# Kernel optimization log

Measured on AMD Instinct MI355X. Metric: run time of the kernel, lower is better.

Reference implementation:

```python
import jax, jax.numpy as jnp
import numpy as np

D = 1024          # d_input_feature
GCN_OUTS = [1024, 512, 256]
DEC_OUTS = [512, 1024, 1024]  # reversed[1:] + [d_input_feature]
EPS = 1e-3        # keras LayerNormalization default epsilon


def _ln(x, gamma, beta):
    m = jnp.mean(x, axis=-1, keepdims=True)
    v = jnp.mean(jnp.square(x - m), axis=-1, keepdims=True)
    return gamma * (x - m) * jax.lax.rsqrt(v + EPS) + beta


def _gcn(x, A, W, b, act):
    # message passing with dense adjacency: act((A @ x) @ W + b)
    h = jnp.einsum('bij,bjd->bid', A, x)
    return act(h @ W + b)


def setup_inputs() -> dict:
    key = jax.random.key(0)
    ks = jax.random.split(key, 40)
    B, DG, DC, NTT = 16384, 772, 100, 128
    inp = {
        't_1': jax.random.randint(ks[0], (B,), 0, NTT),
        'g_1': jax.random.normal(ks[1], (B, DG), jnp.float32),
        'c_1': jax.random.normal(ks[2], (B, DC), jnp.float32),
        'A_1': jax.random.uniform(ks[3], (B, 3, 3), jnp.float32),
        't_2': jax.random.randint(ks[4], (B,), 0, NTT),
        'g_2': jax.random.normal(ks[5], (B, DG), jnp.float32),
        'c_2': jax.random.normal(ks[6], (B, DC), jnp.float32),
        'A_2': jax.random.uniform(ks[7], (B, 3, 3), jnp.float32),
        'embed': jax.random.normal(ks[8], (NTT, D), jnp.float32) * 0.02,
        'Wt': jax.random.normal(ks[9], (D, D), jnp.float32) / np.sqrt(D),
        'bt': jnp.zeros((D,), jnp.float32),
        'Wg': jax.random.normal(ks[10], (DG, D), jnp.float32) / np.sqrt(DG),
        'bg': jnp.zeros((D,), jnp.float32),
        'Wc': jax.random.normal(ks[11], (DC, D), jnp.float32) / np.sqrt(DC),
        'bc': jnp.zeros((D,), jnp.float32),
        'ln_t_g': jnp.ones((D,), jnp.float32), 'ln_t_b': jnp.zeros((D,), jnp.float32),
        'ln_g_g': jnp.ones((D,), jnp.float32), 'ln_g_b': jnp.zeros((D,), jnp.float32),
        'ln_c_g': jnp.ones((D,), jnp.float32), 'ln_c_b': jnp.zeros((D,), jnp.float32),
    }
    d_in = D
    for i, d_out in enumerate(GCN_OUTS):
        inp[f'enc_W{i}'] = jax.random.normal(ks[12 + i], (d_in, d_out), jnp.float32) / np.sqrt(d_in)
        inp[f'enc_b{i}'] = jnp.zeros((d_out,), jnp.float32)
        d_in = d_out
    for i, d_out in enumerate(DEC_OUTS):
        inp[f'dec_W{i}'] = jax.random.normal(ks[20 + i], (d_in, d_out), jnp.float32) / np.sqrt(d_in)
        inp[f'dec_b{i}'] = jnp.zeros((d_out,), jnp.float32)
        d_in = d_out
    return inp


def _branch(t, g, c, embed, Wt, bt, Wg, bg, Wc, bc,
            ln_t_g, ln_t_b, ln_g_g, ln_g_b, ln_c_g, ln_c_b):
    te = embed[t]                               # [B, D]
    te = jax.nn.relu(te @ Wt + bt)
    ge = jax.nn.relu(g @ Wg + bg)
    ce = jax.nn.relu(c @ Wc + bc)
    te = _ln(te, ln_t_g, ln_t_b)
    ge = _ln(ge, ln_g_g, ln_g_b)
    ce = _ln(ce, ln_c_g, ln_c_b)
    return jnp.stack([te, ge, ce], axis=1)      # [B, 3, D]


def _encoder(X, A, enc):
    x = X
    for W, b in enc:
        x = _gcn(x, A, W, b, jax.nn.relu)
    return x


def _decoder(Z, A, dec):
    x = Z
    for W, b in dec:
        x = _gcn(x, A, W, b, jax.nn.silu)       # swish
    return x


def reference(t_1, g_1, c_1, A_1, t_2, g_2, c_2, A_2,
              embed, Wt, bt, Wg, bg, Wc, bc,
              ln_t_g, ln_t_b, ln_g_g, ln_g_b, ln_c_g, ln_c_b,
              enc_W0, enc_b0, enc_W1, enc_b1, enc_W2, enc_b2,
              dec_W0, dec_b0, dec_W1, dec_b1, dec_W2, dec_b2):
    enc = [(enc_W0, enc_b0), (enc_W1, enc_b1), (enc_W2, enc_b2)]
    dec = [(dec_W0, dec_b0), (dec_W1, dec_b1), (dec_W2, dec_b2)]
    bargs = (embed, Wt, bt, Wg, bg, Wc, bc,
             ln_t_g, ln_t_b, ln_g_g, ln_g_b, ln_c_g, ln_c_b)

    X_1 = _branch(t_1, g_1, c_1, *bargs)
    X_2 = _branch(t_2, g_2, c_2, *bargs)
    Z_1 = _encoder(X_1, A_1, enc)
    Z_2 = _encoder(X_2, A_2, enc)
    Z_loss = jnp.square(Z_1 - Z_2)              # [B, 3, 256]

    # GAE reconstruction path (recomputes X per the original code)
    X_h_1 = _decoder(Z_1, A_1, dec)
    X_h_2 = _decoder(Z_2, A_2, dec)
    X_loss = (jnp.square(X_1 - X_h_1) + jnp.square(X_2 - X_h_2)) / 2.0  # [B, 3, D]
    return Z_loss, X_loss
```

## Files before the change

### kernel.cpp

```cpp
#include <hip/hip_runtime.h>


typedef __attribute__((ext_vector_type(8))) short s16x8;
typedef __attribute__((ext_vector_type(4))) short s16x4;
typedef __attribute__((ext_vector_type(4))) float f32x4;

#define DEV static __device__ __forceinline__

DEV float b2f(ushort u) { return __builtin_bit_cast(float, (unsigned)u << 16); }
DEV ushort f2b(float f) {
  unsigned x = __builtin_bit_cast(unsigned, f);
  unsigned r = x + 0x7fffu + ((x >> 16) & 1u);
  return (ushort)(r >> 16);
}

typedef const __attribute__((address_space(1))) void* gas_ptr;
typedef __attribute__((address_space(3))) void* las_ptr;

template<int ACT>
__global__ __launch_bounds__(512, 2) void gemm256(
    const ushort* __restrict__ A, const ushort* __restrict__ BT,
    const float* __restrict__ bias, ushort* __restrict__ C,
    int M, int N, int K)
{
  __shared__ __align__(16) ushort ldsbuf[65536];
  char* Lb = (char*)ldsbuf;

  const int tid = threadIdx.x, lane = tid & 63, w = tid >> 6;
  const int wm = w >> 2, wn = w & 3;

  const int gx  = gridDim.x;
  const int nwg = gx * gridDim.y;
  const int wid = blockIdx.y * gx + blockIdx.x;
  const int q   = nwg >> 3;
  const int Lw  = (wid & 7) * q + (wid >> 3);
  const int bn  = Lw % gx;
  const int bm  = Lw / gx;

  const ushort* Abase = A  + (size_t)bm * 256 * K;
  const ushort* Bbase = BT + (size_t)bn * 256 * K;
  const int T = K >> 6;

  const int srow = w * 8 + (lane >> 3);
  const int scol = (((lane & 7) ^ (lane >> 3)) << 3);

#define STAGE(buf, m, half, Gb, k0)                                          \
  {                                                                          \
    _Pragma("unroll") for (int _j = 0; _j < 2; ++_j) {                       \
      const ushort* _src = (Gb) + (size_t)((half)*128 + _j*64 + srow) * K    \
                           + (k0) + scol;                                    \
      ushort* _dst = (ushort*)(Lb + ((buf)*2 + (m)) * 32768                  \
                               + ((half)*128 + _j*64 + w*8) * 128);          \
      __builtin_amdgcn_global_load_lds((gas_ptr)_src, (las_ptr)_dst, 16,0,0);\
    }                                                                        \
  }

  const int lr = lane & 15, lk = lane >> 4;

#define READ_A(dst, c, mh)                                                   \
  _Pragma("unroll") for (int _i = 0; _i < 4; ++_i)                           \
    _Pragma("unroll") for (int _kk = 0; _kk < 2; ++_kk) {                    \
      const int _r   = (mh)*128 + wm*64 + _i*16 + lr;                        \
      const int _cbb = _kk*64 + lk*16;                                       \
      dst[_i][_kk] = *(const s16x8*)(Lb + ((c)*2 + 0)*32768 + _r*128         \
                                     + (_cbb ^ ((_r & 7) << 4)));            \
    }
#define READ_B(dst, c, nh)                                                   \
  _Pragma("unroll") for (int _p = 0; _p < 2; ++_p)                           \
    _Pragma("unroll") for (int _kk = 0; _kk < 2; ++_kk) {                    \
      const int _r   = (nh)*128 + wn*32 + _p*16 + lr;                        \
      const int _cbb = _kk*64 + lk*16;                                       \
      dst[_p][_kk] = *(const s16x8*)(Lb + ((c)*2 + 1)*32768 + _r*128         \
                                     + (_cbb ^ ((_r & 7) << 4)));            \
    }

#define MFMA_Q(mh, nh)                                                       \
  _Pragma("unroll") for (int _i = 0; _i < 4; ++_i)                           \
    _Pragma("unroll") for (int _p = 0; _p < 2; ++_p)                         \
      _Pragma("unroll") for (int _kk = 0; _kk < 2; ++_kk)                    \
        acc[(mh)*4 + _i][(nh)*2 + _p] =                                      \
            __builtin_amdgcn_mfma_f32_16x16x32_bf16(                         \
                af[_i][_kk], bf[_p][_kk], acc[(mh)*4 + _i][(nh)*2 + _p],     \
                0, 0, 0);

#define MIDBAR  do { __builtin_amdgcn_s_barrier();                           \
                     asm volatile("s_waitcnt lgkmcnt(0)" ::: "memory");      \
                     __builtin_amdgcn_sched_barrier(0);                      \
                     __builtin_amdgcn_s_setprio(1); } while (0)
#define ENDBAR  do { __builtin_amdgcn_s_setprio(0);                          \
                     __builtin_amdgcn_s_barrier(); } while (0)

  f32x4 acc[8][4];
  #pragma unroll
  for (int i = 0; i < 8; ++i)
    #pragma unroll
    for (int j = 0; j < 4; ++j) acc[i][j] = f32x4{0.f, 0.f, 0.f, 0.f};

  STAGE(0, 0, 0, Abase, 0);
  STAGE(0, 1, 0, Bbase, 0);
  STAGE(0, 1, 1, Bbase, 0);
  STAGE(0, 0, 1, Abase, 0);
  STAGE(1, 0, 0, Abase, 64);
  STAGE(1, 1, 1, Bbase, 64);
  STAGE(1, 0, 1, Abase, 64);
  asm volatile("s_waitcnt vmcnt(6)" ::: "memory");
  __builtin_amdgcn_s_barrier();

  for (int t = 0; t < T; ++t) {
    const int cbuf = t & 1, nbuf = cbuf ^ 1;
    const int k1 = ((t + 1 < T) ? t + 1 : t + 1 - T) * 64;
    const int k2 = ((t + 2 < T) ? t + 2 : t + 2 - T) * 64;
    s16x8 af[4][2], bf[2][2];
    READ_A(af, cbuf, 0);
    READ_B(bf, cbuf, 0);
    STAGE(nbuf, 1, 0, Bbase, k1);
    asm volatile("s_waitcnt lgkmcnt(8)" ::: "memory");
    MIDBAR; MFMA_Q(0, 0); ENDBAR;
    READ_B(bf, cbuf, 1);
    STAGE(cbuf, 0, 0, Abase, k2);
    MIDBAR; MFMA_Q(0, 1); ENDBAR;
    READ_A(af, cbuf, 1);
    STAGE(cbuf, 1, 1, Bbase, k2);
    MIDBAR; MFMA_Q(1, 1); ENDBAR;
    READ_B(bf, cbuf, 0);
    STAGE(cbuf, 0, 1, Abase, k2);
    MIDBAR; MFMA_Q(1, 0);
    __builtin_amdgcn_s_setprio(0);
    asm volatile("s_waitcnt vmcnt(6)" ::: "memory");
    __builtin_amdgcn_s_barrier();
  }

  const int row0 = bm * 256, col0 = bn * 256;
  #pragma unroll
  for (int mi = 0; mi < 8; ++mi) {
    const int row = row0 + (mi >> 2) * 128 + wm * 64 + (mi & 3) * 16 + lk * 4;
    #pragma unroll
    for (int ni = 0; ni < 4; ++ni) {
      const int col = col0 + (ni >> 1) * 128 + wn * 32 + (ni & 1) * 16 + lr;
      const float bv = bias[col];
      #pragma unroll
      for (int r = 0; r < 4; ++r) {
        float v = acc[mi][ni][r] + bv;
        if (ACT == 0) v = fmaxf(v, 0.f);
        else          v = v / (1.f + __expf(-v));
        C[(size_t)(row + r) * N + col] = f2b(v);
      }
    }
  }
#undef STAGE
#undef READ_A
#undef READ_B
#undef MFMA_Q
#undef MIDBAR
#undef ENDBAR
}

template<int ACT>
__global__ __launch_bounds__(256, 2) void gemm128(
    const ushort* __restrict__ A, const ushort* __restrict__ BT,
    const float* __restrict__ bias, ushort* __restrict__ C,
    int M, int N, int K)
{
  __shared__ __align__(16) ushort lds[32768];
  char* Lb = (char*)lds;

  const int tid = threadIdx.x, lane = tid & 63;
  const int w = tid >> 6;
  const int wm = w >> 1, wn = w & 1;

  const int gx  = gridDim.x;
  const int nwg = gx * gridDim.y;
  const int wid = blockIdx.y * gx + blockIdx.x;
  const int q   = nwg >> 3;
  const int Lw  = (wid & 7) * q + (wid >> 3);
  const int bn  = Lw % gx;
  const int bm  = Lw / gx;

  const ushort* Abase = A  + (size_t)bm * 128 * K;
  const ushort* Bbase = BT + (size_t)bn * 128 * K;
  const int T = K >> 6;

  const int srow = tid >> 3;
  const int scol = (((tid & 7) ^ (srow & 7)) << 3);

#define STAGE128(buf, k0)                                                    \
  {                                                                          \
    _Pragma("unroll") for (int _j = 0; _j < 4; ++_j)                         \
      __builtin_amdgcn_global_load_lds(                                      \
          (gas_ptr)(Abase + (size_t)(_j * 32 + srow) * K + (k0) + scol),     \
          (las_ptr)(Lb + (buf) + _j * 4096 + tid * 16), 16, 0, 0);           \
    _Pragma("unroll") for (int _j = 0; _j < 4; ++_j)                         \
      __builtin_amdgcn_global_load_lds(                                      \
          (gas_ptr)(Bbase + (size_t)(_j * 32 + srow) * K + (k0) + scol),     \
          (las_ptr)(Lb + (buf) + 16384 + _j * 4096 + tid * 16), 16, 0, 0);   \
  }

  const int lr = lane & 15, lk = lane >> 4;

  f32x4 acc[4][4];
  #pragma unroll
  for (int f = 0; f < 4; ++f)
    #pragma unroll
    for (int p = 0; p < 4; ++p) acc[f][p] = f32x4{0.f, 0.f, 0.f, 0.f};

  STAGE128(0, 0);
  __syncthreads();

  for (int t = 0; t < T; ++t) {
    const int cb = (t & 1) << 15, nb = cb ^ 32768;
    if (t + 1 < T) STAGE128(nb, (t + 1) << 6);

    s16x8 af[4][2], bf[4][2];
    #pragma unroll
    for (int f = 0; f < 4; ++f)
      #pragma unroll
      for (int kk = 0; kk < 2; ++kk) {
        const int r = wm * 64 + f * 16 + lr;
        af[f][kk] = *(const s16x8*)(Lb + cb + r * 128
                                    + ((kk * 64 + lk * 16) ^ ((r & 7) << 4)));
      }
    #pragma unroll
    for (int p = 0; p < 4; ++p)
      #pragma unroll
      for (int kk = 0; kk < 2; ++kk) {
        const int r = wn * 64 + p * 16 + lr;
        bf[p][kk] = *(const s16x8*)(Lb + cb + 16384 + r * 128
                                    + ((kk * 64 + lk * 16) ^ ((r & 7) << 4)));
      }
    #pragma unroll
    for (int f = 0; f < 4; ++f)
      #pragma unroll
      for (int p = 0; p < 4; ++p)
        #pragma unroll
        for (int kk = 0; kk < 2; ++kk)
          acc[f][p] = __builtin_amdgcn_mfma_f32_16x16x32_bf16(
              af[f][kk], bf[p][kk], acc[f][p], 0, 0, 0);

    __syncthreads();
  }

  const int row0 = bm * 128 + wm * 64;
  const int col0 = bn * 128 + wn * 64;
  #pragma unroll
  for (int f = 0; f < 4; ++f) {
    const int row = row0 + f * 16 + lk * 4;
    #pragma unroll
    for (int p = 0; p < 4; ++p) {
      const int col = col0 + p * 16 + lr;
      const float bv = bias[col];
      #pragma unroll
      for (int r = 0; r < 4; ++r) {
        float v = acc[f][p][r] + bv;
        if (ACT == 0) v = fmaxf(v, 0.f);
        else          v = v / (1.f + __expf(-v));
        C[(size_t)(row + r) * N + col] = f2b(v);
      }
    }
  }
#undef STAGE128
}

__global__ void trans_conv(const float* __restrict__ W, ushort* __restrict__ WT,
                           int K, int N, int Kpad)
{
  __shared__ float tile[32][33];
  const int n0 = blockIdx.x * 32, k0 = blockIdx.y * 32;
  const int tx = threadIdx.x, ty = threadIdx.y;
  #pragma unroll
  for (int r = 0; r < 4; r++) {
    const int k = k0 + ty + r * 8;
    tile[ty + r * 8][tx] = (k < K) ? W[(size_t)k * N + n0 + tx] : 0.f;
  }
  __syncthreads();
  #pragma unroll
  for (int r = 0; r < 4; r++) {
    const int n = n0 + ty + r * 8;
    WT[(size_t)n * Kpad + k0 + tx] = f2b(tile[tx][ty + r * 8]);
  }
}

__global__ void conv_pad(const float* __restrict__ in, ushort* __restrict__ out,
                         int R, int Cin, int Cpad)
{
  const int gid = blockIdx.x * 256 + threadIdx.x;
  if (gid >= R * Cpad) return;
  const int r = gid / Cpad, c = gid - r * Cpad;
  out[gid] = (c < Cin) ? f2b(in[(size_t)r * Cin + c]) : (ushort)0;
}

DEV void ln_row(const ushort* __restrict__ in, const float* __restrict__ gamma,
                const float* __restrict__ beta, ushort* __restrict__ outp,
                int tid, float* red)
{
  s16x4 v = *(const s16x4*)&in[tid * 4];
  const float x0 = b2f((ushort)v[0]), x1 = b2f((ushort)v[1]);
  const float x2 = b2f((ushort)v[2]), x3 = b2f((ushort)v[3]);
  float s = x0 + x1 + x2 + x3;
  float qq = x0 * x0 + x1 * x1 + x2 * x2 + x3 * x3;
  #pragma unroll
  for (int o = 32; o > 0; o >>= 1) { s += __shfl_down(s, o); qq += __shfl_down(qq, o); }
  const int wv = tid >> 6, lane = tid & 63;
  __syncthreads();
  if (lane == 0) { red[wv] = s; red[4 + wv] = qq; }
  __syncthreads();
  s  = red[0] + red[1] + red[2] + red[3];
  qq = red[4] + red[5] + red[6] + red[7];
  const float m   = s * (1.f / 1024.f);
  const float var = qq * (1.f / 1024.f) - m * m;
  const float rs  = rsqrtf(var + 1e-3f);
  const int c = tid * 4;
  s16x4 o;
  o[0] = (short)f2b(gamma[c + 0] * ((x0 - m) * rs) + beta[c + 0]);
  o[1] = (short)f2b(gamma[c + 1] * ((x1 - m) * rs) + beta[c + 1]);
  o[2] = (short)f2b(gamma[c + 2] * ((x2 - m) * rs) + beta[c + 2]);
  o[3] = (short)f2b(gamma[c + 3] * ((x3 - m) * rs) + beta[c + 3]);
  *(s16x4*)&outp[c] = o;
}

__global__ void ln_te(const ushort* __restrict__ in, const float* __restrict__ g,
                      const float* __restrict__ b, ushort* __restrict__ out)
{
  __shared__ float red[8];
  ln_row(in + (size_t)blockIdx.x * 1024, g, b,
         out + (size_t)blockIdx.x * 1024, threadIdx.x, red);
}

__global__ void assembleX(const int* __restrict__ t, const ushort* __restrict__ tetab,
                          const ushort* __restrict__ ge, const ushort* __restrict__ ce,
                          const float* __restrict__ gG, const float* __restrict__ gB,
                          const float* __restrict__ cG, const float* __restrict__ cB,
                          ushort* __restrict__ X)
{
  __shared__ float red[8];
  const int b = blockIdx.x, tid = threadIdx.x;
  const int tt = t[b];
  *(s16x4*)&X[(size_t)b * 3072 + tid * 4] =
      *(const s16x4*)&tetab[(size_t)tt * 1024 + tid * 4];
  ln_row(ge + (size_t)b * 1024, gG, gB, X + (size_t)b * 3072 + 1024, tid, red);
  ln_row(ce + (size_t)b * 1024, cG, cB, X + (size_t)b * 3072 + 2048, tid, red);
}

__global__ void mix3(const ushort* __restrict__ x, const float* __restrict__ Am,
                     ushort* __restrict__ out, int d, int lg, int nB)
{
  const int gid = blockIdx.x * 256 + threadIdx.x;
  const int b = gid >> lg;
  if (b >= nB) return;
  const int c8 = (gid & ((1 << lg) - 1)) << 3;
  const ushort* xb = x   + (size_t)b * 3 * d + c8;
  ushort*       ob = out + (size_t)b * 3 * d + c8;
  s16x8 x0 = *(const s16x8*)xb;
  s16x8 x1 = *(const s16x8*)(xb + d);
  s16x8 x2 = *(const s16x8*)(xb + 2 * d);
  float f0[8], f1[8], f2[8];
  #pragma unroll
  for (int e = 0; e < 8; e++) {
    f0[e] = b2f((ushort)x0[e]); f1[e] = b2f((ushort)x1[e]); f2[e] = b2f((ushort)x2[e]);
  }
  const float* Ab = Am + (size_t)b * 9;
  #pragma unroll
  for (int j = 0; j < 3; j++) {
    const float a0 = Ab[j * 3], a1 = Ab[j * 3 + 1], a2 = Ab[j * 3 + 2];
    s16x8 o;
    #pragma unroll
    for (int e = 0; e < 8; e++)
      o[e] = (short)f2b(a0 * f0[e] + a1 * f1[e] + a2 * f2[e]);
    *(s16x8*)(ob + j * d) = o;
  }
}

__global__ void zloss_k(const ushort* __restrict__ z1, const ushort* __restrict__ z2,
                        float* __restrict__ out, int n8)
{
  const int gid = blockIdx.x * 256 + threadIdx.x;
  if (gid >= n8) return;
  const size_t i = (size_t)gid * 8;
  s16x8 a = *(const s16x8*)&z1[i];
  s16x8 b = *(const s16x8*)&z2[i];
  f32x4 o0, o1;
  #pragma unroll
  for (int e = 0; e < 4; e++) {
    float d0 = b2f((ushort)a[e]) - b2f((ushort)b[e]);
    float d1 = b2f((ushort)a[e + 4]) - b2f((ushort)b[e + 4]);
    o0[e] = d0 * d0; o1[e] = d1 * d1;
  }
  *(f32x4*)&out[i] = o0; *(f32x4*)&out[i + 4] = o1;
}

__global__ void xloss2_k(const ushort* __restrict__ X1, const ushort* __restrict__ Xh1,
                         const ushort* __restrict__ X2, const ushort* __restrict__ Xh2,
                         float* __restrict__ out, int n8)
{
  const int gid = blockIdx.x * 256 + threadIdx.x;
  if (gid >= n8) return;
  const size_t i = (size_t)gid * 8;
  s16x8 a1 = *(const s16x8*)&X1[i];
  s16x8 h1 = *(const s16x8*)&Xh1[i];
  s16x8 a2 = *(const s16x8*)&X2[i];
  s16x8 h2 = *(const s16x8*)&Xh2[i];
  f32x4 o0, o1;
  #pragma unroll
  for (int e = 0; e < 4; e++) {
    float d1a = b2f((ushort)a1[e])     - b2f((ushort)h1[e]);
    float d2a = b2f((ushort)a2[e])     - b2f((ushort)h2[e]);
    float d1b = b2f((ushort)a1[e + 4]) - b2f((ushort)h1[e + 4]);
    float d2b = b2f((ushort)a2[e + 4]) - b2f((ushort)h2[e + 4]);
    o0[e] = 0.5f * (d1a * d1a + d2a * d2a);
    o1[e] = 0.5f * (d1b * d1b + d2b * d2b);
  }
  *(f32x4*)&out[i] = o0; *(f32x4*)&out[i + 4] = o1;
}

template<int ADD>
__global__ void xloss_k(const ushort* __restrict__ X, const ushort* __restrict__ Xh,
                        float* __restrict__ out, int n8)
{
  const int gid = blockIdx.x * 256 + threadIdx.x;
  if (gid >= n8) return;
  const size_t i = (size_t)gid * 8;
  s16x8 a = *(const s16x8*)&X[i];
  s16x8 b = *(const s16x8*)&Xh[i];
  f32x4 o0, o1;
  #pragma unroll
  for (int e = 0; e < 4; e++) {
    float d0 = b2f((ushort)a[e]) - b2f((ushort)b[e]);
    float d1 = b2f((ushort)a[e + 4]) - b2f((ushort)b[e + 4]);
    o0[e] = 0.5f * d0 * d0; o1[e] = 0.5f * d1 * d1;
  }
  if (ADD) {
    f32x4 p0 = *(const f32x4*)&out[i];
    f32x4 p1 = *(const f32x4*)&out[i + 4];
    #pragma unroll
    for (int e = 0; e < 4; e++) { o0[e] += p0[e]; o1[e] += p1[e]; }
  }
  *(f32x4*)&out[i] = o0; *(f32x4*)&out[i + 4] = o1;
}

extern "C" void kernel_launch(void* const* d_in, const int* in_sizes, int n_in,
                              void* d_out, int out_size, void* d_ws, size_t ws_size,
                              hipStream_t stream)
{
  const int B = 16384, S = 3 * B;
  const int*   t1 = (const int*)d_in[0];
  const float* g1 = (const float*)d_in[1];
  const float* c1 = (const float*)d_in[2];
  const float* A1 = (const float*)d_in[3];
  const int*   t2 = (const int*)d_in[4];
  const float* g2 = (const float*)d_in[5];
  const float* c2 = (const float*)d_in[6];
  const float* A2 = (const float*)d_in[7];
  const float* embed = (const float*)d_in[8];
  const float* Wt = (const float*)d_in[9];  const float* bt = (const float*)d_in[10];
  const float* Wg = (const float*)d_in[11]; const float* bg = (const float*)d_in[12];
  const float* Wc = (const float*)d_in[13]; const float* bc = (const float*)d_in[14];
  const float* lntg = (const float*)d_in[15]; const float* lntb = (const float*)d_in[16];
  const float* lngg = (const float*)d_in[17]; const float* lngb = (const float*)d_in[18];
  const float* lncg = (const float*)d_in[19]; const float* lncb = (const float*)d_in[20];
  const float* eW0 = (const float*)d_in[21]; const float* eb0 = (const float*)d_in[22];
  const float* eW1 = (const float*)d_in[23]; const float* eb1 = (const float*)d_in[24];
  const float* eW2 = (const float*)d_in[25]; const float* eb2 = (const float*)d_in[26];
  const float* dW0 = (const float*)d_in[27]; const float* db0 = (const float*)d_in[28];
  const float* dW1 = (const float*)d_in[29]; const float* db1 = (const float*)d_in[30];
  const float* dW2 = (const float*)d_in[31]; const float* db2 = (const float*)d_in[32];
  float* out = (float*)d_out;
  (void)in_sizes; (void)n_in; (void)out_size;

  char* ws = (char*)d_ws; size_t off = 0;
  auto alloc = [&](size_t bytes) -> void* {
    void* p = ws + off; off += (bytes + 255) & ~(size_t)255; return p;
  };
  ushort* WtT  = (ushort*)alloc((size_t)1024 * 1024 * 2);
  ushort* WgT  = (ushort*)alloc((size_t)1024 * 896 * 2);
  ushort* WcT  = (ushort*)alloc((size_t)1024 * 128 * 2);
  ushort* E0T  = (ushort*)alloc((size_t)1024 * 1024 * 2);
  ushort* E1T  = (ushort*)alloc((size_t)512 * 1024 * 2);
  ushort* E2T  = (ushort*)alloc((size_t)256 * 512 * 2);
  ushort* D0T  = (ushort*)alloc((size_t)512 * 256 * 2);
  ushort* D1T  = (ushort*)alloc((size_t)1024 * 512 * 2);
  ushort* D2T  = (ushort*)alloc((size_t)1024 * 1024 * 2);
  ushort* embB = (ushort*)alloc((size_t)128 * 1024 * 2);
  ushort* teraw= (ushort*)alloc((size_t)128 * 1024 * 2);
  ushort* tetab= (ushort*)alloc((size_t)128 * 1024 * 2);
  ushort* gB[2] = {(ushort*)alloc((size_t)B * 896 * 2), (ushort*)alloc((size_t)B * 896 * 2)};
  ushort* cB[2] = {(ushort*)alloc((size_t)B * 128 * 2), (ushort*)alloc((size_t)B * 128 * 2)};
  ushort* zB[2] = {(ushort*)alloc((size_t)S * 256 * 2), (ushort*)alloc((size_t)S * 256 * 2)};
  ushort* Xb0 = (ushort*)alloc((size_t)S * 1024 * 2);
  ushort* b0  = (ushort*)alloc((size_t)S * 1024 * 2);
  ushort* b1  = (ushort*)alloc((size_t)S * 1024 * 2);
  ushort* Xb1 = (ushort*)alloc((size_t)S * 1024 * 2);
  ushort* xh1 = (ushort*)alloc((size_t)S * 1024 * 2);
  const bool fused = (off <= ws_size);

  const dim3 TB(32, 8);
  trans_conv<<<dim3(32, 32), TB, 0, stream>>>(Wt,  WtT, 1024, 1024, 1024);
  trans_conv<<<dim3(32, 28), TB, 0, stream>>>(Wg,  WgT,  772, 1024,  896);
  trans_conv<<<dim3(32,  4), TB, 0, stream>>>(Wc,  WcT,  100, 1024,  128);
  trans_conv<<<dim3(32, 32), TB, 0, stream>>>(eW0, E0T, 1024, 1024, 1024);
  trans_conv<<<dim3(16, 32), TB, 0, stream>>>(eW1, E1T, 1024,  512, 1024);
  trans_conv<<<dim3( 8, 16), TB, 0, stream>>>(eW2, E2T,  512,  256,  512);
  trans_conv<<<dim3(16,  8), TB, 0, stream>>>(dW0, D0T,  256,  512,  256);
  trans_conv<<<dim3(32, 16), TB, 0, stream>>>(dW1, D1T,  512, 1024,  512);
  trans_conv<<<dim3(32, 32), TB, 0, stream>>>(dW2, D2T, 1024, 1024, 1024);
  conv_pad<<<512, 256, 0, stream>>>(embed, embB, 128, 1024, 1024);
  conv_pad<<<(B * 896 + 255) / 256, 256, 0, stream>>>(g1, gB[0], B, 772, 896);
  conv_pad<<<(B * 896 + 255) / 256, 256, 0, stream>>>(g2, gB[1], B, 772, 896);
  conv_pad<<<B * 128 / 256, 256, 0, stream>>>(c1, cB[0], B, 100, 128);
  conv_pad<<<B * 128 / 256, 256, 0, stream>>>(c2, cB[1], B, 100, 128);
  gemm128<0><<<dim3(8, 1), 256, 0, stream>>>(embB, WtT, bt, teraw, 128, 1024, 1024);
  ln_te<<<128, 256, 0, stream>>>(teraw, lntg, lntb, tetab);

  const size_t ZLEN = (size_t)S * 256;
  const int n8x = S * 1024 / 8;
  for (int br = 0; br < 2; ++br) {
    const int*   t    = br ? t2 : t1;
    const float* Aadj = br ? A2 : A1;
    ushort* Xb = (fused && br) ? Xb1 : Xb0;
    gemm256<0><<<dim3(4, B / 256), 512, 0, stream>>>(gB[br], WgT, bg, b0, B, 1024, 896);
    gemm128<0><<<dim3(8, B / 128), 256, 0, stream>>>(cB[br], WcT, bc, b1, B, 1024, 128);
    assembleX<<<B, 256, 0, stream>>>(t, tetab, b0, b1, lngg, lngb, lncg, lncb, Xb);
    mix3<<<(B << 7) / 256, 256, 0, stream>>>(Xb, Aadj, b0, 1024, 7, B);
    gemm256<0><<<dim3(4, S / 256), 512, 0, stream>>>(b0, E0T, eb0, b1, S, 1024, 1024);
    mix3<<<(B << 7) / 256, 256, 0, stream>>>(b1, Aadj, b0, 1024, 7, B);
    gemm256<0><<<dim3(2, S / 256), 512, 0, stream>>>(b0, E1T, eb1, b1, S, 512, 1024);
    mix3<<<(B << 6) / 256, 256, 0, stream>>>(b1, Aadj, b0, 512, 6, B);
    gemm128<0><<<dim3(2, S / 128), 256, 0, stream>>>(b0, E2T, eb2, zB[br], S, 256, 512);
    mix3<<<(B << 5) / 256, 256, 0, stream>>>(zB[br], Aadj, b0, 256, 5, B);
    gemm128<1><<<dim3(4, S / 128), 256, 0, stream>>>(b0, D0T, db0, b1, S, 512, 256);
    mix3<<<(B << 6) / 256, 256, 0, stream>>>(b1, Aadj, b0, 512, 6, B);
    gemm256<1><<<dim3(4, S / 256), 512, 0, stream>>>(b0, D1T, db1, b1, S, 1024, 512);
    mix3<<<(B << 7) / 256, 256, 0, stream>>>(b1, Aadj, b0, 1024, 7, B);
    if (fused) {
      ushort* xh = br ? b1 : xh1;
      gemm256<1><<<dim3(4, S / 256), 512, 0, stream>>>(b0, D2T, db2, xh, S, 1024, 1024);
      if (br)
        xloss2_k<<<n8x / 256, 256, 0, stream>>>(Xb0, xh1, Xb1, b1, out + ZLEN, n8x);
    } else {
      gemm256<1><<<dim3(4, S / 256), 512, 0, stream>>>(b0, D2T, db2, b1, S, 1024, 1024);
      if (br == 0)
        xloss_k<0><<<n8x / 256, 256, 0, stream>>>(Xb0, b1, out + ZLEN, n8x);
      else
        xloss_k<1><<<n8x / 256, 256, 0, stream>>>(Xb0, b1, out + ZLEN, n8x);
    }
  }
  zloss_k<<<S * 256 / 8 / 256, 256, 0, stream>>>(zB[0], zB[1], out, S * 256 / 8);
}
```

Measured before the change: 1.506 ms.

## Batch both branches into one pipeline with doubled row count

Concatenates the two input branches along the batch dimension so each GEMM, mix3 and assembleX launch processes both branches at once, with per-row selection of t and A by a split index. This halves the number of launches and doubles the grid size per GEMM, which improves occupancy and tail utilization on the smaller layers. The cost is doubling the workspace footprint, with a fallback to the per-branch path when the workspace is too small.

Result: no change. 1.487 ms (-1.2%).

```diff
diff --git a/kernel.cpp b/kernel.cpp
--- a/kernel.cpp
+++ b/kernel.cpp
@@ -325,7 +325,8 @@
          out + (size_t)blockIdx.x * 1024, threadIdx.x, red);
 }
 
-__global__ void assembleX(const int* __restrict__ t, const ushort* __restrict__ tetab,
+__global__ void assembleX(const int* __restrict__ ta, const int* __restrict__ tb,
+                          int split, const ushort* __restrict__ tetab,
                           const ushort* __restrict__ ge, const ushort* __restrict__ ce,
                           const float* __restrict__ gG, const float* __restrict__ gB,
                           const float* __restrict__ cG, const float* __restrict__ cB,
@@ -333,15 +334,16 @@
 {
   __shared__ float red[8];
   const int b = blockIdx.x, tid = threadIdx.x;
-  const int tt = t[b];
+  const int tt = (b < split) ? ta[b] : tb[b - split];
   *(s16x4*)&X[(size_t)b * 3072 + tid * 4] =
       *(const s16x4*)&tetab[(size_t)tt * 1024 + tid * 4];
   ln_row(ge + (size_t)b * 1024, gG, gB, X + (size_t)b * 3072 + 1024, tid, red);
   ln_row(ce + (size_t)b * 1024, cG, cB, X + (size_t)b * 3072 + 2048, tid, red);
 }
 
-__global__ void mix3(const ushort* __restrict__ x, const float* __restrict__ Am,
-                     ushort* __restrict__ out, int d, int lg, int nB)
+__global__ void mix3(const ushort* __restrict__ x,
+                     const float* __restrict__ Aa, const float* __restrict__ Ab2,
+                     int split, ushort* __restrict__ out, int d, int lg, int nB)
 {
   const int gid = blockIdx.x * 256 + threadIdx.x;
   const int b = gid >> lg;
@@ -357,7 +359,8 @@
   for (int e = 0; e < 8; e++) {
     f0[e] = b2f((ushort)x0[e]); f1[e] = b2f((ushort)x1[e]); f2[e] = b2f((ushort)x2[e]);
   }
-  const float* Ab = Am + (size_t)b * 9;
+  const float* Ab = (b < split) ? (Aa + (size_t)b * 9)
+                                : (Ab2 + (size_t)(b - split) * 9);
   #pragma unroll
   for (int j = 0; j < 3; j++) {
     const float a0 = Ab[j * 3], a1 = Ab[j * 3 + 1], a2 = Ab[j * 3 + 2];
@@ -407,31 +410,6 @@
     float d2b = b2f((ushort)a2[e + 4]) - b2f((ushort)h2[e + 4]);
     o0[e] = 0.5f * (d1a * d1a + d2a * d2a);
     o1[e] = 0.5f * (d1b * d1b + d2b * d2b);
-  }
-  *(f32x4*)&out[i] = o0; *(f32x4*)&out[i + 4] = o1;
-}
-
-template<int ADD>
-__global__ void xloss_k(const ushort* __restrict__ X, const ushort* __restrict__ Xh,
-                        float* __restrict__ out, int n8)
-{
-  const int gid = blockIdx.x * 256 + threadIdx.x;
-  if (gid >= n8) return;
-  const size_t i = (size_t)gid * 8;
-  s16x8 a = *(const s16x8*)&X[i];
-  s16x8 b = *(const s16x8*)&Xh[i];
-  f32x4 o0, o1;
-  #pragma unroll
-  for (int e = 0; e < 4; e++) {
-    float d0 = b2f((ushort)a[e]) - b2f((ushort)b[e]);
-    float d1 = b2f((ushort)a[e + 4]) - b2f((ushort)b[e + 4]);
-    o0[e] = 0.5f * d0 * d0; o1[e] = 0.5f * d1 * d1;
-  }
-  if (ADD) {
-    f32x4 p0 = *(const f32x4*)&out[i];
-    f32x4 p1 = *(const f32x4*)&out[i + 4];
-    #pragma unroll
-    for (int e = 0; e < 4; e++) { o0[e] += p0[e]; o1[e] += p1[e]; }
   }
   *(f32x4*)&out[i] = o0; *(f32x4*)&out[i + 4] = o1;
 }
@@ -481,15 +459,31 @@
   ushort* embB = (ushort*)alloc((size_t)128 * 1024 * 2);
   ushort* teraw= (ushort*)alloc((size_t)128 * 1024 * 2);
   ushort* tetab= (ushort*)alloc((size_t)128 * 1024 * 2);
-  ushort* gB[2] = {(ushort*)alloc((size_t)B * 896 * 2), (ushort*)alloc((size_t)B * 896 * 2)};
-  ushort* cB[2] = {(ushort*)alloc((size_t)B * 128 * 2), (ushort*)alloc((size_t)B * 128 * 2)};
-  ushort* zB[2] = {(ushort*)alloc((size_t)S * 256 * 2), (ushort*)alloc((size_t)S * 256 * 2)};
-  ushort* Xb0 = (ushort*)alloc((size_t)S * 1024 * 2);
-  ushort* b0  = (ushort*)alloc((size_t)S * 1024 * 2);
-  ushort* b1  = (ushort*)alloc((size_t)S * 1024 * 2);
-  ushort* Xb1 = (ushort*)alloc((size_t)S * 1024 * 2);
-  ushort* xh1 = (ushort*)alloc((size_t)S * 1024 * 2);
-  const bool fused = (off <= ws_size);
+  const size_t woff = off;
+
+  ushort* G  = (ushort*)alloc((size_t)2 * B * 896 * 2);
+  ushort* Cc = (ushort*)alloc((size_t)2 * B * 128 * 2);
+  ushort* Z  = (ushort*)alloc((size_t)2 * S * 256 * 2);
+  ushort* Xs = (ushort*)alloc((size_t)2 * S * 1024 * 2);
+  ushort* b0 = (ushort*)alloc((size_t)2 * S * 1024 * 2);
+  ushort* b1 = (ushort*)alloc((size_t)2 * S * 1024 * 2);
+  const bool merged = (off <= ws_size);
+
+  ushort *fG[2], *fC[2], *fZ[2], *fX[2], *fb0, *fb1, *fxh;
+  if (!merged) {
+    off = woff;
+    fG[0] = (ushort*)alloc((size_t)B * 896 * 2);
+    fG[1] = (ushort*)alloc((size_t)B * 896 * 2);
+    fC[0] = (ushort*)alloc((size_t)B * 128 * 2);
+    fC[1] = (ushort*)alloc((size_t)B * 128 * 2);
+    fZ[0] = (ushort*)alloc((size_t)S * 256 * 2);
+    fZ[1] = (ushort*)alloc((size_t)S * 256 * 2);
+    fX[0] = (ushort*)alloc((size_t)S * 1024 * 2);
+    fX[1] = (ushort*)alloc((size_t)S * 1024 * 2);
+    fb0   = (ushort*)alloc((size_t)S * 1024 * 2);
+    fb1   = (ushort*)alloc((size_t)S * 1024 * 2);
+    fxh   = (ushort*)alloc((size_t)S * 1024 * 2);
+  }
 
   const dim3 TB(32, 8);
   trans_conv<<<dim3(32, 32), TB, 0, stream>>>(Wt,  WtT, 1024, 1024, 1024);
@@ -502,45 +496,53 @@
   trans_conv<<<dim3(32, 16), TB, 0, stream>>>(dW1, D1T,  512, 1024,  512);
   trans_conv<<<dim3(32, 32), TB, 0, stream>>>(dW2, D2T, 1024, 1024, 1024);
   conv_pad<<<512, 256, 0, stream>>>(embed, embB, 128, 1024, 1024);
-  conv_pad<<<(B * 896 + 255) / 256, 256, 0, stream>>>(g1, gB[0], B, 772, 896);
-  conv_pad<<<(B * 896 + 255) / 256, 256, 0, stream>>>(g2, gB[1], B, 772, 896);
-  conv_pad<<<B * 128 / 256, 256, 0, stream>>>(c1, cB[0], B, 100, 128);
-  conv_pad<<<B * 128 / 256, 256, 0, stream>>>(c2, cB[1], B, 100, 128);
   gemm128<0><<<dim3(8, 1), 256, 0, stream>>>(embB, WtT, bt, teraw, 128, 1024, 1024);
   ln_te<<<128, 256, 0, stream>>>(teraw, lntg, lntb, tetab);
 
   const size_t ZLEN = (size_t)S * 256;
   const int n8x = S * 1024 / 8;
-  for (int br = 0; br < 2; ++br) {
-    const int*   t    = br ? t2 : t1;
-    const float* Aadj = br ? A2 : A1;
-    ushort* Xb = (fused && br) ? Xb1 : Xb0;
-    gemm256<0><<<dim3(4, B / 256), 512, 0, stream>>>(gB[br], WgT, bg, b0, B, 1024, 896);
-    gemm128<0><<<dim3(8, B / 128), 256, 0, stream>>>(cB[br], WcT, bc, b1, B, 1024, 128);
-    assembleX<<<B, 256, 0, stream>>>(t, tetab, b0, b1, lngg, lngb, lncg, lncb, Xb);
-    mix3<<<(B << 7) / 256, 256, 0, stream>>>(Xb, Aadj, b0, 1024, 7, B);
-    gemm256<0><<<dim3(4, S / 256), 512, 0, stream>>>(b0, E0T, eb0, b1, S, 1024, 1024);
-    mix3<<<(B << 7) / 256, 256, 0, stream>>>(b1, Aadj, b0, 1024, 7, B);
-    gemm256<0><<<dim3(2, S / 256), 512, 0, stream>>>(b0, E1T, eb1, b1, S, 512, 1024);
-    mix3<<<(B << 6) / 256, 256, 0, stream>>>(b1, Aadj, b0, 512, 6, B);
-    gemm128<0><<<dim3(2, S / 128), 256, 0, stream>>>(b0, E2T, eb2, zB[br], S, 256, 512);
-    mix3<<<(B << 5) / 256, 256, 0, stream>>>(zB[br], Aadj, b0, 256, 5, B);
-    gemm128<1><<<dim3(4, S / 128), 256, 0, stream>>>(b0, D0T, db0, b1, S, 512, 256);
-    mix3<<<(B << 6) / 256, 256, 0, stream>>>(b1, Aadj, b0, 512, 6, B);
-    gemm256<1><<<dim3(4, S / 256), 512, 0, stream>>>(b0, D1T, db1, b1, S, 1024, 512);
-    mix3<<<(B << 7) / 256, 256, 0, stream>>>(b1, Aadj, b0, 1024, 7, B);
-    if (fused) {
-      ushort* xh = br ? b1 : xh1;
-      gemm256<1><<<dim3(4, S / 256), 512, 0, stream>>>(b0, D2T, db2, xh, S, 1024, 1024);
-      if (br)
-        xloss2_k<<<n8x / 256, 256, 0, stream>>>(Xb0, xh1, Xb1, b1, out + ZLEN, n8x);
-    } else {
-      gemm256<1><<<dim3(4, S / 256), 512, 0, stream>>>(b0, D2T, db2, b1, S, 1024, 1024);
-      if (br == 0)
-        xloss_k<0><<<n8x / 256, 256, 0, stream>>>(Xb0, b1, out + ZLEN, n8x);
-      else
-        xloss_k<1><<<n8x / 256, 256, 0, stream>>>(Xb0, b1, out + ZLEN, n8x);
+
+  auto pipeline = [&](ushort* Gp, ushort* Cp, const int* ta, const int* tb,
+                      const float* Aa, const float* Ab2, int split, int nS,
+                      ushort* Xp, ushort* p0, ushort* p1, ushort* Zp, ushort* xh) {
+    const int Ms = nS * 3;
+    gemm256<0><<<dim3(4, nS / 256), 512, 0, stream>>>(Gp, WgT, bg, p0, nS, 1024, 896);
+    gemm128<0><<<dim3(8, nS / 128), 256, 0, stream>>>(Cp, WcT, bc, p1, nS, 1024, 128);
+    assembleX<<<nS, 256, 0, stream>>>(ta, tb, split, tetab, p0, p1,
+                                      lngg, lngb, lncg, lncb, Xp);
+    mix3<<<(nS << 7) / 256, 256, 0, stream>>>(Xp, Aa, Ab2, split, p0, 1024, 7, nS);
+    gemm256<0><<<dim3(4, Ms / 256), 512, 0, stream>>>(p0, E0T, eb0, p1, Ms, 1024, 1024);
+    mix3<<<(nS << 7) / 256, 256, 0, stream>>>(p1, Aa, Ab2, split, p0, 1024, 7, nS);
+    gemm256<0><<<dim3(2, Ms / 256), 512, 0, stream>>>(p0, E1T, eb1, p1, Ms, 512, 1024);
+    mix3<<<(nS << 6) / 256, 256, 0, stream>>>(p1, Aa, Ab2, split, p0, 512, 6, nS);
+    gemm128<0><<<dim3(2, Ms / 128), 256, 0, stream>>>(p0, E2T, eb2, Zp, Ms, 256, 512);
+    mix3<<<(nS << 5) / 256, 256, 0, stream>>>(Zp, Aa, Ab2, split, p0, 256, 5, nS);
+    gemm128<1><<<dim3(4, Ms / 128), 256, 0, stream>>>(p0, D0T, db0, p1, Ms, 512, 256);
+    mix3<<<(nS << 6) / 256, 256, 0, stream>>>(p1, Aa, Ab2, split, p0, 512, 6, nS);
+    gemm256<1><<<dim3(4, Ms / 256), 512, 0, stream>>>(p0, D1T, db1, p1, Ms, 1024, 512);
+    mix3<<<(nS << 7) / 256, 256, 0, stream>>>(p1, Aa, Ab2, split, p0, 1024, 7, nS);
+    gemm256<1><<<dim3(4, Ms / 256), 512, 0, stream>>>(p0, D2T, db2, xh, Ms, 1024, 1024);
+  };
+
+  if (merged) {
+    conv_pad<<<(B * 896 + 255) / 256, 256, 0, stream>>>(g1, G, B, 772, 896);
+    conv_pad<<<(B * 896 + 255) / 256, 256, 0, stream>>>(g2, G + (size_t)B * 896, B, 772, 896);
+    conv_pad<<<B * 128 / 256, 256, 0, stream>>>(c1, Cc, B, 100, 128);
+    conv_pad<<<B * 128 / 256, 256, 0, stream>>>(c2, Cc + (size_t)B * 128, B, 100, 128);
+    pipeline(G, Cc, t1, t2, A1, A2, B, 2 * B, Xs, b0, b1, Z, b1);
+    xloss2_k<<<n8x / 256, 256, 0, stream>>>(
+        Xs, b1, Xs + (size_t)S * 1024, b1 + (size_t)S * 1024, out + ZLEN, n8x);
+    zloss_k<<<(int)(ZLEN / 8 / 256), 256, 0, stream>>>(Z, Z + ZLEN, out, (int)(ZLEN / 8));
+  } else {
+    for (int br = 0; br < 2; ++br) {
+      conv_pad<<<(B * 896 + 255) / 256, 256, 0, stream>>>(br ? g2 : g1, fG[br], B, 772, 896);
+      conv_pad<<<B * 128 / 256, 256, 0, stream>>>(br ? c2 : c1, fC[br], B, 100, 128);
+      const int*   t    = br ? t2 : t1;
+      const float* Aadj = br ? A2 : A1;
+      pipeline(fG[br], fC[br], t, t, Aadj, Aadj, B, B,
+               fX[br], fb0, fb1, fZ[br], br ? fb1 : fxh);
     }
-  }
-  zloss_k<<<S * 256 / 8 / 256, 256, 0, stream>>>(zB[0], zB[1], out, S * 256 / 8);
-}
+    xloss2_k<<<n8x / 256, 256, 0, stream>>>(fX[0], fxh, fX[1], fb1, out + ZLEN, n8x);
+    zloss_k<<<(int)(ZLEN / 8 / 256), 256, 0, stream>>>(fZ[0], fZ[1], out, (int)(ZLEN / 8));
+  }
+}
```
